# Performance work log

Measured on AMD Instinct MI355X. Metric: run time of the kernel, lower is better.

## Reference

```python
import jax, jax.numpy as jnp
import numpy as np

TOP_K = 2
NUM_EXPERTS = 64


def setup_inputs() -> dict:
    key = jax.random.key(0)
    k1, k2, k3 = jax.random.split(key, 3)
    T, D, E = 16384, 2048, NUM_EXPERTS
    x = jax.random.normal(k1, (T, D), dtype=jnp.float32)
    # gate projection weight (the _forward of the concrete router)
    w_gate = jax.random.normal(k2, (D, E), dtype=jnp.float32) * (1.0 / np.sqrt(D))
    # gate.perturbation(scores.shape, NORMAL): additive Gaussian noise, materialized for determinism
    noise = jax.random.normal(k3, (T, E), dtype=jnp.float32)
    return {"x": x, "w_gate": w_gate, "noise": noise}


def reference(x, w_gate, noise):
    T, E = x.shape[0], w_gate.shape[1]
    # _forward: expert scores [T, E]
    scores = x @ w_gate
    # gate.compute on perturbed scores: softmax -> top-k -> renormalized gates
    probs = jax.nn.softmax(scores + noise, axis=-1)
    topk_vals, topk_idx = jax.lax.top_k(probs, TOP_K)          # [T, k]
    gates = topk_vals / jnp.sum(topk_vals, axis=-1, keepdims=True)
    # combine tensor [T, E]: gate weight scattered to the chosen experts
    rows = jnp.arange(T)[:, None]                               # [T, 1]
    combine = jnp.zeros((T, E), dtype=gates.dtype).at[rows, topk_idx].add(gates)
    # _track_expert_activations: scatter_add of ones per selected expert column
    expert_activation = jnp.zeros((E,), dtype=jnp.float32).at[topk_idx.ravel()].add(1.0)
    return combine, topk_idx, gates, expert_activation
```

## Files before the change

kernel.cpp:

```cpp
#include <hip/hip_runtime.h>
#include <math.h>

#define T_TOKENS 16384
#define DIM      2048
#define NEXP     64
#define TOPK     2

#define OFF_COMBINE 0
#define OFF_IDX     (T_TOKENS * NEXP)
#define OFF_GATES   (OFF_IDX + T_TOKENS * TOPK)
#define OFF_ACT     (OFF_GATES + T_TOKENS * TOPK)

#define PSTR 68
#define WT_PLANE (NEXP * DIM)

#define NKC   4
#define KC    (DIM / NKC)
#define NSTEP (KC / 32)

typedef __attribute__((ext_vector_type(8))) short  short8;
typedef __attribute__((ext_vector_type(4))) float  f32x4;

#define MFMA16(a, b, c) __builtin_amdgcn_mfma_f32_16x16x32_bf16((a), (b), (c), 0, 0, 0)

__device__ __align__(16) unsigned short g_wt[3 * WT_PLANE];

__global__ void wsplit_kernel(const float* __restrict__ w,
                              float* __restrict__ out) {
    const int tid = threadIdx.x;
    const int e   = blockIdx.x;
    if (e == 0 && tid < NEXP) out[OFF_ACT + tid] = 0.0f;

    const int k0 = tid * 8;
    short8 hs, ms, ls;
    #pragma unroll
    for (int i = 0; i < 8; ++i) {
        const float v = w[(size_t)(k0 + i) * NEXP + e];
        const unsigned int bv = __builtin_bit_cast(unsigned int, v);
        const unsigned int hb = bv & 0xFFFF0000u;
        const float r1 = v - __builtin_bit_cast(float, hb);
        const unsigned int r1b = __builtin_bit_cast(unsigned int, r1);
        const unsigned int mb = r1b & 0xFFFF0000u;
        const float r2 = r1 - __builtin_bit_cast(float, mb);
        const unsigned int lb = __builtin_bit_cast(unsigned int, r2);
        hs[i] = (short)(hb >> 16);
        ms[i] = (short)(mb >> 16);
        ls[i] = (short)(lb >> 16);
    }
    *reinterpret_cast<short8*>(&g_wt[(size_t)e * DIM + k0])                = hs;
    *reinterpret_cast<short8*>(&g_wt[(size_t)e * DIM + k0 + WT_PLANE])     = ms;
    *reinterpret_cast<short8*>(&g_wt[(size_t)e * DIM + k0 + 2 * WT_PLANE]) = ls;
}

__device__ __forceinline__ void gload_lds16(const float* g, float* s) {
    __builtin_amdgcn_global_load_lds(
        (const __attribute__((address_space(1))) void*)g,
        (__attribute__((address_space(3))) void*)s, 16, 0, 0);
}

__device__ __forceinline__ void split8(const float4 a, const float4 b,
                                       short8& ah, short8& am, short8& al) {
    float v[8] = {a.x, a.y, a.z, a.w, b.x, b.y, b.z, b.w};
    #pragma unroll
    for (int i = 0; i < 8; ++i) {
        const unsigned int bv = __builtin_bit_cast(unsigned int, v[i]);
        const unsigned int hb = bv & 0xFFFF0000u;
        const float r1 = v[i] - __builtin_bit_cast(float, hb);
        const unsigned int r1b = __builtin_bit_cast(unsigned int, r1);
        const unsigned int mb = r1b & 0xFFFF0000u;
        const float r2 = r1 - __builtin_bit_cast(float, mb);
        const unsigned int lb = __builtin_bit_cast(unsigned int, r2);
        ah[i] = (short)(hb >> 16);
        am[i] = (short)(mb >> 16);
        al[i] = (short)(lb >> 16);
    }
}

__global__ __launch_bounds__(512, 2)
void router_kernel(const float* __restrict__ x,
                   const float* __restrict__ noise,
                   float* __restrict__ out) {
    __shared__ __align__(16) float pool[NKC * 64 * PSTR];
    __shared__ __align__(16) float nsh[64][PSTR];
    __shared__ float g1s[64], g2s[64];
    __shared__ int   i1s[64], i2s[64];
    __shared__ float bins[NEXP];

    const int tid  = threadIdx.x;
    const int l    = tid & 63;
    const int wv   = __builtin_amdgcn_readfirstlane(tid >> 6);
    const int lrow = l & 15;
    const int lk   = l >> 4;
    const int mt   = wv & 1;
    const int kc   = wv >> 1;
    const int brow = blockIdx.x * 64;

    if (tid < NEXP) bins[tid] = 0.0f;

    #pragma unroll
    for (int i = 0; i < 2; ++i) {
        const int idx = tid + i * 512;
        const int r = idx >> 4, c = (idx & 15) * 4;
        *reinterpret_cast<float4*>(&nsh[r][c]) =
            *reinterpret_cast<const float4*>(noise + (size_t)(brow + r) * NEXP + c);
    }

    float* xs = pool + wv * 2048;
    const float* xg0 = x + (size_t)(brow + mt * 32 + lrow) * DIM + kc * KC + lk * 8;
    const float* xg1 = x + (size_t)(brow + mt * 32 + 16 + lrow) * DIM + kc * KC + lk * 8;

    const unsigned short* wb[4];
    #pragma unroll
    for (int n = 0; n < 4; ++n)
        wb[n] = g_wt + (size_t)(n * 16 + lrow) * DIM + kc * KC + lk * 8;

    f32x4 acc[2][4];
    #pragma unroll
    for (int f = 0; f < 2; ++f)
        #pragma unroll
        for (int n = 0; n < 4; ++n) acc[f][n] = (f32x4){0.f, 0.f, 0.f, 0.f};

#define STAGE(b, t) do {                                              \
        const int _ko = (t) * 32;                                     \
        gload_lds16(xg0 + _ko,     xs + (b) * 1024 + 0 * 256);        \
        gload_lds16(xg0 + _ko + 4, xs + (b) * 1024 + 1 * 256);        \
        gload_lds16(xg1 + _ko,     xs + (b) * 1024 + 2 * 256);        \
        gload_lds16(xg1 + _ko + 4, xs + (b) * 1024 + 3 * 256);        \
    } while (0)

    STAGE(0, 0);

    #pragma unroll 2
    for (int s = 0; s < NSTEP; ++s) {
        const int b = s & 1;

        asm volatile("s_waitcnt vmcnt(0)" ::: "memory");

        const float4 xa0 = *reinterpret_cast<const float4*>(xs + b * 1024 +       l * 4);
        const float4 xa1 = *reinterpret_cast<const float4*>(xs + b * 1024 + 256 + l * 4);
        const float4 xa2 = *reinterpret_cast<const float4*>(xs + b * 1024 + 512 + l * 4);
        const float4 xa3 = *reinterpret_cast<const float4*>(xs + b * 1024 + 768 + l * 4);

        const int tn = (s + 1 < NSTEP) ? (s + 1) : s;
        STAGE(b ^ 1, tn);

        short8 Wh[4], Wm[4], Wl[4];
        #pragma unroll
        for (int n = 0; n < 4; ++n) {
            const unsigned short* p = wb[n] + s * 32;
            Wh[n] = *reinterpret_cast<const short8*>(p);
            Wm[n] = *reinterpret_cast<const short8*>(p + WT_PLANE);
            Wl[n] = *reinterpret_cast<const short8*>(p + 2 * WT_PLANE);
        }

        short8 a0h, a0m, a0l, a1h, a1m, a1l;
        split8(xa0, xa1, a0h, a0m, a0l);
        split8(xa2, xa3, a1h, a1m, a1l);

        #pragma unroll
        for (int n = 0; n < 4; ++n) {
            acc[0][n] = MFMA16(a0h, Wh[n], acc[0][n]);
            acc[0][n] = MFMA16(a0h, Wm[n], acc[0][n]);
            acc[0][n] = MFMA16(a0m, Wh[n], acc[0][n]);
            acc[0][n] = MFMA16(a0h, Wl[n], acc[0][n]);
            acc[0][n] = MFMA16(a0m, Wm[n], acc[0][n]);
            acc[0][n] = MFMA16(a0l, Wh[n], acc[0][n]);
            acc[1][n] = MFMA16(a1h, Wh[n], acc[1][n]);
            acc[1][n] = MFMA16(a1h, Wm[n], acc[1][n]);
            acc[1][n] = MFMA16(a1m, Wh[n], acc[1][n]);
            acc[1][n] = MFMA16(a1h, Wl[n], acc[1][n]);
            acc[1][n] = MFMA16(a1m, Wm[n], acc[1][n]);
            acc[1][n] = MFMA16(a1l, Wh[n], acc[1][n]);
        }
    }
#undef STAGE

    __syncthreads();

    #pragma unroll
    for (int f = 0; f < 2; ++f)
        #pragma unroll
        for (int n = 0; n < 4; ++n)
            #pragma unroll
            for (int j = 0; j < 4; ++j)
                pool[((size_t)kc * 64 + (mt * 32 + f * 16 + lk * 4 + j)) * PSTR
                     + (n * 16 + lrow)] = acc[f][n][j];
    __syncthreads();

    if (wv == 0) {
        const int r   = l;
        const int row = brow + r;
        float m1 = -1e30f, m2 = -1e30f;
        int i1 = 0, i2 = 0;
        #pragma unroll
        for (int j = 0; j < NEXP; j += 4) {
            float4 s4       = *reinterpret_cast<const float4*>(&pool[(0 * 64 + r) * PSTR + j]);
            const float4 p1 = *reinterpret_cast<const float4*>(&pool[(1 * 64 + r) * PSTR + j]);
            const float4 p2 = *reinterpret_cast<const float4*>(&pool[(2 * 64 + r) * PSTR + j]);
            const float4 p3 = *reinterpret_cast<const float4*>(&pool[(3 * 64 + r) * PSTR + j]);
            const float4 nv = *reinterpret_cast<const float4*>(&nsh[r][j]);
            s4.x += p1.x + p2.x + p3.x + nv.x;
            s4.y += p1.y + p2.y + p3.y + nv.y;
            s4.z += p1.z + p2.z + p3.z + nv.z;
            s4.w += p1.w + p2.w + p3.w + nv.w;
            if (s4.x > m1) { m2 = m1; i2 = i1; m1 = s4.x; i1 = j + 0; } else if (s4.x > m2) { m2 = s4.x; i2 = j + 0; }
            if (s4.y > m1) { m2 = m1; i2 = i1; m1 = s4.y; i1 = j + 1; } else if (s4.y > m2) { m2 = s4.y; i2 = j + 1; }
            if (s4.z > m1) { m2 = m1; i2 = i1; m1 = s4.z; i1 = j + 2; } else if (s4.z > m2) { m2 = s4.z; i2 = j + 2; }
            if (s4.w > m1) { m2 = m1; i2 = i1; m1 = s4.w; i1 = j + 3; } else if (s4.w > m2) { m2 = s4.w; i2 = j + 3; }
        }

        const float t  = expf(m2 - m1);
        const float g1 = 1.0f / (1.0f + t);
        const float g2 = 1.0f - g1;

        out[OFF_IDX + row * 2 + 0]   = (float)i1;
        out[OFF_IDX + row * 2 + 1]   = (float)i2;
        out[OFF_GATES + row * 2 + 0] = g1;
        out[OFF_GATES + row * 2 + 1] = g2;

        g1s[r] = g1; g2s[r] = g2; i1s[r] = i1; i2s[r] = i2;
        atomicAdd(&bins[i1], 1.0f);
        atomicAdd(&bins[i2], 1.0f);
    }
    __syncthreads();

    #pragma unroll
    for (int i = 0; i < 2; ++i) {
        const int idx = tid + i * 512;
        const int r = idx >> 4, c = (idx & 15) * 4;
        const int   a  = i1s[r], b = i2s[r];
        const float ga = g1s[r], gb = g2s[r];
        float4 v;
        v.x = (c + 0 == a) ? ga : (c + 0 == b) ? gb : 0.0f;
        v.y = (c + 1 == a) ? ga : (c + 1 == b) ? gb : 0.0f;
        v.z = (c + 2 == a) ? ga : (c + 2 == b) ? gb : 0.0f;
        v.w = (c + 3 == a) ? ga : (c + 3 == b) ? gb : 0.0f;
        *reinterpret_cast<float4*>(
            out + OFF_COMBINE + (size_t)(brow + r) * NEXP + c) = v;
    }

    if (tid < NEXP) {
        const float v = bins[tid];
        if (v != 0.0f) atomicAdd(out + OFF_ACT + tid, v);
    }
}

extern "C" void kernel_launch(void* const* d_in, const int* in_sizes, int n_in,
                              void* d_out, int out_size, void* d_ws, size_t ws_size,
                              hipStream_t stream) {
    const float* x     = (const float*)d_in[0];
    const float* wg    = (const float*)d_in[1];
    const float* noise = (const float*)d_in[2];
    float* out = (float*)d_out;

    wsplit_kernel<<<NEXP, 256, 0, stream>>>(wg, out);
    router_kernel<<<T_TOKENS / 64, 512, 0, stream>>>(x, noise, out);
}
```

Baseline: 251.5 us.

## Stage split weights in LDS and tile 32 tokens per block over full K

Replaces the split-K scheme (64 tokens per block, four K-chunks reduced through shared memory) with 32-token blocks of 256 threads that walk the full K dimension. Both the x tile and the three bf16 weight planes are now double-buffered in LDS with async global-to-LDS loads and XOR-style swizzles, so each wave reads weights from LDS instead of straight from global memory. This removes the cross-chunk partial-sum reduction and doubles the grid size. The cost is a block-wide barrier on every K step and shorter per-wave MFMA chains, which can expose load latency.

Result: no change. 255.5 us (+1.6%).

```diff
diff --git a/kernel.cpp b/kernel.cpp
--- a/kernel.cpp
+++ b/kernel.cpp
@@ -11,12 +11,11 @@
 #define OFF_GATES   (OFF_IDX + T_TOKENS * TOPK)
 #define OFF_ACT     (OFF_GATES + T_TOKENS * TOPK)
 
-#define PSTR 68
 #define WT_PLANE (NEXP * DIM)
 
-#define NKC   4
-#define KC    (DIM / NKC)
-#define NSTEP (KC / 32)
+#define BT    32
+#define BK    32
+#define NSTEP (DIM / BK)
 
 typedef __attribute__((ext_vector_type(8))) short  short8;
 typedef __attribute__((ext_vector_type(4))) float  f32x4;
@@ -52,7 +51,7 @@
     *reinterpret_cast<short8*>(&g_wt[(size_t)e * DIM + k0 + 2 * WT_PLANE]) = ls;
 }
 
-__device__ __forceinline__ void gload_lds16(const float* g, float* s) {
+__device__ __forceinline__ void gload_lds16(const void* g, void* s) {
     __builtin_amdgcn_global_load_lds(
         (const __attribute__((address_space(1))) void*)g,
         (__attribute__((address_space(3))) void*)s, 16, 0, 0);
@@ -76,14 +75,16 @@
     }
 }
 
-__global__ __launch_bounds__(512, 2)
+__global__ __launch_bounds__(256, 2)
 void router_kernel(const float* __restrict__ x,
                    const float* __restrict__ noise,
                    float* __restrict__ out) {
-    __shared__ __align__(16) float pool[NKC * 64 * PSTR];
-    __shared__ __align__(16) float nsh[64][PSTR];
-    __shared__ float g1s[64], g2s[64];
-    __shared__ int   i1s[64], i2s[64];
+    __shared__ __align__(16) float          aS[2][BT * BK];
+    __shared__ __align__(16) unsigned short wS[2][3 * NEXP * BK];
+    __shared__ float scores[BT][68];
+    __shared__ float nshs[BT][68];
+    __shared__ float g1s[BT], g2s[BT];
+    __shared__ int   i1s[BT], i2s[BT];
     __shared__ float bins[NEXP];
 
     const int tid  = threadIdx.x;
@@ -91,118 +92,107 @@
     const int wv   = __builtin_amdgcn_readfirstlane(tid >> 6);
     const int lrow = l & 15;
     const int lk   = l >> 4;
-    const int mt   = wv & 1;
-    const int kc   = wv >> 1;
-    const int brow = blockIdx.x * 64;
+    const int brow = blockIdx.x * BT;
 
     if (tid < NEXP) bins[tid] = 0.0f;
 
     #pragma unroll
     for (int i = 0; i < 2; ++i) {
-        const int idx = tid + i * 512;
+        const int idx = tid + i * 256;
         const int r = idx >> 4, c = (idx & 15) * 4;
-        *reinterpret_cast<float4*>(&nsh[r][c]) =
+        *reinterpret_cast<float4*>(&nshs[r][c]) =
             *reinterpret_cast<const float4*>(noise + (size_t)(brow + r) * NEXP + c);
     }
 
-    float* xs = pool + wv * 2048;
-    const float* xg0 = x + (size_t)(brow + mt * 32 + lrow) * DIM + kc * KC + lk * 8;
-    const float* xg1 = x + (size_t)(brow + mt * 32 + 16 + lrow) * DIM + kc * KC + lk * 8;
-
-    const unsigned short* wb[4];
-    #pragma unroll
-    for (int n = 0; n < 4; ++n)
-        wb[n] = g_wt + (size_t)(n * 16 + lrow) * DIM + kc * KC + lk * 8;
-
-    f32x4 acc[2][4];
-    #pragma unroll
-    for (int f = 0; f < 2; ++f)
-        #pragma unroll
-        for (int n = 0; n < 4; ++n) acc[f][n] = (f32x4){0.f, 0.f, 0.f, 0.f};
-
-#define STAGE(b, t) do {                                              \
-        const int _ko = (t) * 32;                                     \
-        gload_lds16(xg0 + _ko,     xs + (b) * 1024 + 0 * 256);        \
-        gload_lds16(xg0 + _ko + 4, xs + (b) * 1024 + 1 * 256);        \
-        gload_lds16(xg1 + _ko,     xs + (b) * 1024 + 2 * 256);        \
-        gload_lds16(xg1 + _ko + 4, xs + (b) * 1024 + 3 * 256);        \
+    const int arow = wv * 8 + (l >> 3);
+    const int agch = ((l & 7) - arow) & 7;
+    const float* asrc = x + (size_t)(brow + arow) * DIM + agch * 4;
+    float* adst = &aS[0][0] + wv * 256;
+
+    const unsigned short* wsrc[3];
+    unsigned short* wdst[3];
+    #pragma unroll
+    for (int t = 0; t < 3; ++t) {
+        const int op = wv * 3 + t;
+        const int p  = op >> 2, q = op & 3;
+        const int e  = q * 16 + (l >> 2);
+        const int gch = ((l & 3) - e) & 3;
+        wsrc[t] = g_wt + (size_t)p * WT_PLANE + (size_t)e * DIM + gch * 8;
+        wdst[t] = &wS[0][0] + p * 2048 + q * 512;
+    }
+
+#define STAGE(bf, ss) do {                                            \
+        gload_lds16(asrc + (ss) * BK,     adst    + (bf) * 1024);     \
+        gload_lds16(wsrc[0] + (ss) * BK,  wdst[0] + (bf) * 6144);     \
+        gload_lds16(wsrc[1] + (ss) * BK,  wdst[1] + (bf) * 6144);     \
+        gload_lds16(wsrc[2] + (ss) * BK,  wdst[2] + (bf) * 6144);     \
     } while (0)
 
+    const int af = wv & 1;
+    const int n0 = (wv >> 1) * 2;
+    const int ar = af * 16 + lrow;
+    const int ac0 = ((2 * lk + ar) & 7) * 4;
+    const int ac1 = ((2 * lk + 1 + ar) & 7) * 4;
+    int woff[2];
+    #pragma unroll
+    for (int n = 0; n < 2; ++n) {
+        const int e = (n0 + n) * 16 + lrow;
+        woff[n] = e * 32 + ((lk + e) & 3) * 8;
+    }
+
+    f32x4 acc[2];
+    acc[0] = (f32x4){0.f, 0.f, 0.f, 0.f};
+    acc[1] = acc[0];
+
     STAGE(0, 0);
+    __syncthreads();
 
     #pragma unroll 2
     for (int s = 0; s < NSTEP; ++s) {
         const int b = s & 1;
-
-        asm volatile("s_waitcnt vmcnt(0)" ::: "memory");
-
-        const float4 xa0 = *reinterpret_cast<const float4*>(xs + b * 1024 +       l * 4);
-        const float4 xa1 = *reinterpret_cast<const float4*>(xs + b * 1024 + 256 + l * 4);
-        const float4 xa2 = *reinterpret_cast<const float4*>(xs + b * 1024 + 512 + l * 4);
-        const float4 xa3 = *reinterpret_cast<const float4*>(xs + b * 1024 + 768 + l * 4);
-
-        const int tn = (s + 1 < NSTEP) ? (s + 1) : s;
-        STAGE(b ^ 1, tn);
-
-        short8 Wh[4], Wm[4], Wl[4];
+        const int sn = (s + 1 < NSTEP) ? (s + 1) : s;
+        STAGE(b ^ 1, sn);
+
+        const float* ab = &aS[b][ar * 32];
+        const float4 xa0 = *reinterpret_cast<const float4*>(ab + ac0);
+        const float4 xa1 = *reinterpret_cast<const float4*>(ab + ac1);
+        short8 ah, am, al;
+        split8(xa0, xa1, ah, am, al);
+
+        const unsigned short* wbuf = &wS[b][0];
         #pragma unroll
-        for (int n = 0; n < 4; ++n) {
-            const unsigned short* p = wb[n] + s * 32;
-            Wh[n] = *reinterpret_cast<const short8*>(p);
-            Wm[n] = *reinterpret_cast<const short8*>(p + WT_PLANE);
-            Wl[n] = *reinterpret_cast<const short8*>(p + 2 * WT_PLANE);
+        for (int n = 0; n < 2; ++n) {
+            const short8 Wh = *reinterpret_cast<const short8*>(wbuf +        woff[n]);
+            const short8 Wm = *reinterpret_cast<const short8*>(wbuf + 2048 + woff[n]);
+            const short8 Wl = *reinterpret_cast<const short8*>(wbuf + 4096 + woff[n]);
+            acc[n] = MFMA16(ah, Wh, acc[n]);
+            acc[n] = MFMA16(ah, Wm, acc[n]);
+            acc[n] = MFMA16(am, Wh, acc[n]);
+            acc[n] = MFMA16(ah, Wl, acc[n]);
+            acc[n] = MFMA16(am, Wm, acc[n]);
+            acc[n] = MFMA16(al, Wh, acc[n]);
         }
-
-        short8 a0h, a0m, a0l, a1h, a1m, a1l;
-        split8(xa0, xa1, a0h, a0m, a0l);
-        split8(xa2, xa3, a1h, a1m, a1l);
-
+        __syncthreads();
+    }
+#undef STAGE
+
+    #pragma unroll
+    for (int n = 0; n < 2; ++n)
         #pragma unroll
-        for (int n = 0; n < 4; ++n) {
-            acc[0][n] = MFMA16(a0h, Wh[n], acc[0][n]);
-            acc[0][n] = MFMA16(a0h, Wm[n], acc[0][n]);
-            acc[0][n] = MFMA16(a0m, Wh[n], acc[0][n]);
-            acc[0][n] = MFMA16(a0h, Wl[n], acc[0][n]);
-            acc[0][n] = MFMA16(a0m, Wm[n], acc[0][n]);
-            acc[0][n] = MFMA16(a0l, Wh[n], acc[0][n]);
-            acc[1][n] = MFMA16(a1h, Wh[n], acc[1][n]);
-            acc[1][n] = MFMA16(a1h, Wm[n], acc[1][n]);
-            acc[1][n] = MFMA16(a1m, Wh[n], acc[1][n]);
-            acc[1][n] = MFMA16(a1h, Wl[n], acc[1][n]);
-            acc[1][n] = MFMA16(a1m, Wm[n], acc[1][n]);
-            acc[1][n] = MFMA16(a1l, Wh[n], acc[1][n]);
-        }
-    }
-#undef STAGE
-
+        for (int j = 0; j < 4; ++j)
+            scores[af * 16 + lk * 4 + j][(n0 + n) * 16 + lrow] = acc[n][j];
     __syncthreads();
 
-    #pragma unroll
-    for (int f = 0; f < 2; ++f)
-        #pragma unroll
-        for (int n = 0; n < 4; ++n)
-            #pragma unroll
-            for (int j = 0; j < 4; ++j)
-                pool[((size_t)kc * 64 + (mt * 32 + f * 16 + lk * 4 + j)) * PSTR
-                     + (n * 16 + lrow)] = acc[f][n][j];
-    __syncthreads();
-
-    if (wv == 0) {
-        const int r   = l;
+    if (tid < BT) {
+        const int r   = tid;
         const int row = brow + r;
         float m1 = -1e30f, m2 = -1e30f;
         int i1 = 0, i2 = 0;
         #pragma unroll
         for (int j = 0; j < NEXP; j += 4) {
-            float4 s4       = *reinterpret_cast<const float4*>(&pool[(0 * 64 + r) * PSTR + j]);
-            const float4 p1 = *reinterpret_cast<const float4*>(&pool[(1 * 64 + r) * PSTR + j]);
-            const float4 p2 = *reinterpret_cast<const float4*>(&pool[(2 * 64 + r) * PSTR + j]);
-            const float4 p3 = *reinterpret_cast<const float4*>(&pool[(3 * 64 + r) * PSTR + j]);
-            const float4 nv = *reinterpret_cast<const float4*>(&nsh[r][j]);
-            s4.x += p1.x + p2.x + p3.x + nv.x;
-            s4.y += p1.y + p2.y + p3.y + nv.y;
-            s4.z += p1.z + p2.z + p3.z + nv.z;
-            s4.w += p1.w + p2.w + p3.w + nv.w;
+            float4 s4       = *reinterpret_cast<const float4*>(&scores[r][j]);
+            const float4 nv = *reinterpret_cast<const float4*>(&nshs[r][j]);
+            s4.x += nv.x; s4.y += nv.y; s4.z += nv.z; s4.w += nv.w;
             if (s4.x > m1) { m2 = m1; i2 = i1; m1 = s4.x; i1 = j + 0; } else if (s4.x > m2) { m2 = s4.x; i2 = j + 0; }
             if (s4.y > m1) { m2 = m1; i2 = i1; m1 = s4.y; i1 = j + 1; } else if (s4.y > m2) { m2 = s4.y; i2 = j + 1; }
             if (s4.z > m1) { m2 = m1; i2 = i1; m1 = s4.z; i1 = j + 2; } else if (s4.z > m2) { m2 = s4.z; i2 = j + 2; }
@@ -226,7 +216,7 @@
 
     #pragma unroll
     for (int i = 0; i < 2; ++i) {
-        const int idx = tid + i * 512;
+        const int idx = tid + i * 256;
         const int r = idx >> 4, c = (idx & 15) * 4;
         const int   a  = i1s[r], b = i2s[r];
         const float ga = g1s[r], gb = g2s[r];
@@ -254,5 +244,5 @@
     float* out = (float*)d_out;
 
     wsplit_kernel<<<NEXP, 256, 0, stream>>>(wg, out);
-    router_kernel<<<T_TOKENS / 64, 512, 0, stream>>>(x, noise, out);
-}
+    router_kernel<<<T_TOKENS / BT, 256, 0, stream>>>(x, noise, out);
+}
```

## Shrink router blocks to 16 rows with direct register prefetch of x

Applied to the files above, without the earlier changes.

Each block now handles 16 tokens with 4 waves, one K-chunk per wave, instead of 64 tokens with 8 waves. The x tile is prefetched into registers one step ahead instead of being staged through LDS with global_load_lds. This removes the LDS staging and the full vmcnt wait, and adds more blocks and higher occupancy. The cost is four times as many reads of the split bf16 weight planes, since each wave reuses each weight fragment for only one M tile.

New measurement: 298.0 us. 18.5% more time.

```diff
diff --git a/kernel.cpp b/kernel.cpp
--- a/kernel.cpp
+++ b/kernel.cpp
@@ -11,9 +11,9 @@
 #define OFF_GATES   (OFF_IDX + T_TOKENS * TOPK)
 #define OFF_ACT     (OFF_GATES + T_TOKENS * TOPK)
 
-#define PSTR 68
 #define WT_PLANE (NEXP * DIM)
 
+#define GRP   16
 #define NKC   4
 #define KC    (DIM / NKC)
 #define NSTEP (KC / 32)
@@ -52,12 +52,6 @@
     *reinterpret_cast<short8*>(&g_wt[(size_t)e * DIM + k0 + 2 * WT_PLANE]) = ls;
 }
 
-__device__ __forceinline__ void gload_lds16(const float* g, float* s) {
-    __builtin_amdgcn_global_load_lds(
-        (const __attribute__((address_space(1))) void*)g,
-        (__attribute__((address_space(3))) void*)s, 16, 0, 0);
-}
-
 __device__ __forceinline__ void split8(const float4 a, const float4 b,
                                        short8& ah, short8& am, short8& al) {
     float v[8] = {a.x, a.y, a.z, a.w, b.x, b.y, b.z, b.w};
@@ -76,128 +70,113 @@
     }
 }
 
-__global__ __launch_bounds__(512, 2)
+__global__ __launch_bounds__(256, 4)
 void router_kernel(const float* __restrict__ x,
                    const float* __restrict__ noise,
                    float* __restrict__ out) {
-    __shared__ __align__(16) float pool[NKC * 64 * PSTR];
-    __shared__ __align__(16) float nsh[64][PSTR];
-    __shared__ float g1s[64], g2s[64];
-    __shared__ int   i1s[64], i2s[64];
+    __shared__ float part[NKC][GRP][68];
+    __shared__ float nsh[GRP][68];
+    __shared__ float g1s[GRP], g2s[GRP];
+    __shared__ int   i1s[GRP], i2s[GRP];
     __shared__ float bins[NEXP];
 
     const int tid  = threadIdx.x;
     const int l    = tid & 63;
-    const int wv   = __builtin_amdgcn_readfirstlane(tid >> 6);
+    const int kc   = tid >> 6;
     const int lrow = l & 15;
     const int lk   = l >> 4;
-    const int mt   = wv & 1;
-    const int kc   = wv >> 1;
-    const int brow = blockIdx.x * 64;
+    const int brow = blockIdx.x * GRP;
 
     if (tid < NEXP) bins[tid] = 0.0f;
 
-    #pragma unroll
-    for (int i = 0; i < 2; ++i) {
-        const int idx = tid + i * 512;
-        const int r = idx >> 4, c = (idx & 15) * 4;
+    {
+        const int r = tid >> 4, c = (tid & 15) * 4;
         *reinterpret_cast<float4*>(&nsh[r][c]) =
             *reinterpret_cast<const float4*>(noise + (size_t)(brow + r) * NEXP + c);
     }
 
-    float* xs = pool + wv * 2048;
-    const float* xg0 = x + (size_t)(brow + mt * 32 + lrow) * DIM + kc * KC + lk * 8;
-    const float* xg1 = x + (size_t)(brow + mt * 32 + 16 + lrow) * DIM + kc * KC + lk * 8;
-
-    const unsigned short* wb[4];
+    const float* xa = x + (size_t)(brow + lrow) * DIM + kc * KC + lk * 8;
+    const unsigned short* wb0 = g_wt + (size_t)(0 * 16 + lrow) * DIM + kc * KC + lk * 8;
+    const unsigned short* wb1 = g_wt + (size_t)(1 * 16 + lrow) * DIM + kc * KC + lk * 8;
+    const unsigned short* wb2 = g_wt + (size_t)(2 * 16 + lrow) * DIM + kc * KC + lk * 8;
+    const unsigned short* wb3 = g_wt + (size_t)(3 * 16 + lrow) * DIM + kc * KC + lk * 8;
+
+    f32x4 acc[4];
+    #pragma unroll
+    for (int n = 0; n < 4; ++n) acc[n] = (f32x4){0.f, 0.f, 0.f, 0.f};
+
+    float4 A0 = *reinterpret_cast<const float4*>(xa);
+    float4 A1 = *reinterpret_cast<const float4*>(xa + 4);
+
+    #pragma unroll 1
+    for (int s = 0; s < NSTEP; ++s) {
+        const int sn = (s + 1 < NSTEP) ? (s + 1) : s;
+        const float4 N0 = *reinterpret_cast<const float4*>(xa + sn * 32);
+        const float4 N1 = *reinterpret_cast<const float4*>(xa + sn * 32 + 4);
+
+        const int so = s * 32;
+        const short8 Wh0 = *reinterpret_cast<const short8*>(wb0 + so);
+        const short8 Wm0 = *reinterpret_cast<const short8*>(wb0 + so + WT_PLANE);
+        const short8 Wl0 = *reinterpret_cast<const short8*>(wb0 + so + 2 * WT_PLANE);
+        const short8 Wh1 = *reinterpret_cast<const short8*>(wb1 + so);
+        const short8 Wm1 = *reinterpret_cast<const short8*>(wb1 + so + WT_PLANE);
+        const short8 Wl1 = *reinterpret_cast<const short8*>(wb1 + so + 2 * WT_PLANE);
+        const short8 Wh2 = *reinterpret_cast<const short8*>(wb2 + so);
+        const short8 Wm2 = *reinterpret_cast<const short8*>(wb2 + so + WT_PLANE);
+        const short8 Wl2 = *reinterpret_cast<const short8*>(wb2 + so + 2 * WT_PLANE);
+        const short8 Wh3 = *reinterpret_cast<const short8*>(wb3 + so);
+        const short8 Wm3 = *reinterpret_cast<const short8*>(wb3 + so + WT_PLANE);
+        const short8 Wl3 = *reinterpret_cast<const short8*>(wb3 + so + 2 * WT_PLANE);
+
+        short8 ah, am, al;
+        split8(A0, A1, ah, am, al);
+
+        acc[0] = MFMA16(ah, Wh0, acc[0]);
+        acc[0] = MFMA16(ah, Wm0, acc[0]);
+        acc[0] = MFMA16(am, Wh0, acc[0]);
+        acc[0] = MFMA16(ah, Wl0, acc[0]);
+        acc[0] = MFMA16(am, Wm0, acc[0]);
+        acc[0] = MFMA16(al, Wh0, acc[0]);
+        acc[1] = MFMA16(ah, Wh1, acc[1]);
+        acc[1] = MFMA16(ah, Wm1, acc[1]);
+        acc[1] = MFMA16(am, Wh1, acc[1]);
+        acc[1] = MFMA16(ah, Wl1, acc[1]);
+        acc[1] = MFMA16(am, Wm1, acc[1]);
+        acc[1] = MFMA16(al, Wh1, acc[1]);
+        acc[2] = MFMA16(ah, Wh2, acc[2]);
+        acc[2] = MFMA16(ah, Wm2, acc[2]);
+        acc[2] = MFMA16(am, Wh2, acc[2]);
+        acc[2] = MFMA16(ah, Wl2, acc[2]);
+        acc[2] = MFMA16(am, Wm2, acc[2]);
+        acc[2] = MFMA16(al, Wh2, acc[2]);
+        acc[3] = MFMA16(ah, Wh3, acc[3]);
+        acc[3] = MFMA16(ah, Wm3, acc[3]);
+        acc[3] = MFMA16(am, Wh3, acc[3]);
+        acc[3] = MFMA16(ah, Wl3, acc[3]);
+        acc[3] = MFMA16(am, Wm3, acc[3]);
+        acc[3] = MFMA16(al, Wh3, acc[3]);
+
+        A0 = N0; A1 = N1;
+    }
+
     #pragma unroll
     for (int n = 0; n < 4; ++n)
-        wb[n] = g_wt + (size_t)(n * 16 + lrow) * DIM + kc * KC + lk * 8;
-
-    f32x4 acc[2][4];
-    #pragma unroll
-    for (int f = 0; f < 2; ++f)
         #pragma unroll
-        for (int n = 0; n < 4; ++n) acc[f][n] = (f32x4){0.f, 0.f, 0.f, 0.f};
-
-#define STAGE(b, t) do {                                              \
-        const int _ko = (t) * 32;                                     \
-        gload_lds16(xg0 + _ko,     xs + (b) * 1024 + 0 * 256);        \
-        gload_lds16(xg0 + _ko + 4, xs + (b) * 1024 + 1 * 256);        \
-        gload_lds16(xg1 + _ko,     xs + (b) * 1024 + 2 * 256);        \
-        gload_lds16(xg1 + _ko + 4, xs + (b) * 1024 + 3 * 256);        \
-    } while (0)
-
-    STAGE(0, 0);
-
-    #pragma unroll 2
-    for (int s = 0; s < NSTEP; ++s) {
-        const int b = s & 1;
-
-        asm volatile("s_waitcnt vmcnt(0)" ::: "memory");
-
-        const float4 xa0 = *reinterpret_cast<const float4*>(xs + b * 1024 +       l * 4);
-        const float4 xa1 = *reinterpret_cast<const float4*>(xs + b * 1024 + 256 + l * 4);
-        const float4 xa2 = *reinterpret_cast<const float4*>(xs + b * 1024 + 512 + l * 4);
-        const float4 xa3 = *reinterpret_cast<const float4*>(xs + b * 1024 + 768 + l * 4);
-
-        const int tn = (s + 1 < NSTEP) ? (s + 1) : s;
-        STAGE(b ^ 1, tn);
-
-        short8 Wh[4], Wm[4], Wl[4];
-        #pragma unroll
-        for (int n = 0; n < 4; ++n) {
-            const unsigned short* p = wb[n] + s * 32;
-            Wh[n] = *reinterpret_cast<const short8*>(p);
-            Wm[n] = *reinterpret_cast<const short8*>(p + WT_PLANE);
-            Wl[n] = *reinterpret_cast<const short8*>(p + 2 * WT_PLANE);
-        }
-
-        short8 a0h, a0m, a0l, a1h, a1m, a1l;
-        split8(xa0, xa1, a0h, a0m, a0l);
-        split8(xa2, xa3, a1h, a1m, a1l);
-
-        #pragma unroll
-        for (int n = 0; n < 4; ++n) {
-            acc[0][n] = MFMA16(a0h, Wh[n], acc[0][n]);
-            acc[0][n] = MFMA16(a0h, Wm[n], acc[0][n]);
-            acc[0][n] = MFMA16(a0m, Wh[n], acc[0][n]);
-            acc[0][n] = MFMA16(a0h, Wl[n], acc[0][n]);
-            acc[0][n] = MFMA16(a0m, Wm[n], acc[0][n]);
-            acc[0][n] = MFMA16(a0l, Wh[n], acc[0][n]);
-            acc[1][n] = MFMA16(a1h, Wh[n], acc[1][n]);
-            acc[1][n] = MFMA16(a1h, Wm[n], acc[1][n]);
-            acc[1][n] = MFMA16(a1m, Wh[n], acc[1][n]);
-            acc[1][n] = MFMA16(a1h, Wl[n], acc[1][n]);
-            acc[1][n] = MFMA16(a1m, Wm[n], acc[1][n]);
-            acc[1][n] = MFMA16(a1l, Wh[n], acc[1][n]);
-        }
-    }
-#undef STAGE
-
+        for (int j = 0; j < 4; ++j)
+            part[kc][lk * 4 + j][n * 16 + lrow] = acc[n][j];
     __syncthreads();
 
-    #pragma unroll
-    for (int f = 0; f < 2; ++f)
-        #pragma unroll
-        for (int n = 0; n < 4; ++n)
-            #pragma unroll
-            for (int j = 0; j < 4; ++j)
-                pool[((size_t)kc * 64 + (mt * 32 + f * 16 + lk * 4 + j)) * PSTR
-                     + (n * 16 + lrow)] = acc[f][n][j];
-    __syncthreads();
-
-    if (wv == 0) {
-        const int r   = l;
+    if (tid < GRP) {
+        const int r   = tid;
         const int row = brow + r;
         float m1 = -1e30f, m2 = -1e30f;
         int i1 = 0, i2 = 0;
         #pragma unroll
         for (int j = 0; j < NEXP; j += 4) {
-            float4 s4       = *reinterpret_cast<const float4*>(&pool[(0 * 64 + r) * PSTR + j]);
-            const float4 p1 = *reinterpret_cast<const float4*>(&pool[(1 * 64 + r) * PSTR + j]);
-            const float4 p2 = *reinterpret_cast<const float4*>(&pool[(2 * 64 + r) * PSTR + j]);
-            const float4 p3 = *reinterpret_cast<const float4*>(&pool[(3 * 64 + r) * PSTR + j]);
+            float4 s4       = *reinterpret_cast<const float4*>(&part[0][r][j]);
+            const float4 p1 = *reinterpret_cast<const float4*>(&part[1][r][j]);
+            const float4 p2 = *reinterpret_cast<const float4*>(&part[2][r][j]);
+            const float4 p3 = *reinterpret_cast<const float4*>(&part[3][r][j]);
             const float4 nv = *reinterpret_cast<const float4*>(&nsh[r][j]);
             s4.x += p1.x + p2.x + p3.x + nv.x;
             s4.y += p1.y + p2.y + p3.y + nv.y;
@@ -224,10 +203,8 @@
     }
     __syncthreads();
 
-    #pragma unroll
-    for (int i = 0; i < 2; ++i) {
-        const int idx = tid + i * 512;
-        const int r = idx >> 4, c = (idx & 15) * 4;
+    {
+        const int r = tid >> 4, c = (tid & 15) * 4;
         const int   a  = i1s[r], b = i2s[r];
         const float ga = g1s[r], gb = g2s[r];
         float4 v;
@@ -254,5 +231,5 @@
     float* out = (float*)d_out;
 
     wsplit_kernel<<<NEXP, 256, 0, stream>>>(wg, out);
-    router_kernel<<<T_TOKENS / 64, 512, 0, stream>>>(x, noise, out);
-}
+    router_kernel<<<T_TOKENS / GRP, 256, 0, stream>>>(x, noise, out);
+}
```
